# Kernel tuning notes

Hardware: AMD Instinct MI355X
Metric: run time of the kernel (lower is better)

Reference implementation:

```python
import jax, jax.numpy as jnp
import numpy as np

WEIGHT = 1.0  # init kwarg `weight`
BOX = 5      # half-size of the text box in pixels


def setup_inputs() -> dict:
    key = jax.random.key(0)
    k1, k2, k3, k4 = jax.random.split(key, 4)
    B, C, H, W, T = 32, 4, 512, 512, 64
    return {
        "predicted_noise": jax.random.normal(k1, (B, C, H, W), dtype=jnp.float32),
        "target_noise": jax.random.normal(k2, (B, C, H, W), dtype=jnp.float32),
        "text_tokens": jax.random.randint(k3, (B, T), 0, 50000, dtype=jnp.int64),
        "text_positions": jax.random.uniform(k4, (B, T, 2), dtype=jnp.float32),
    }


def _text_mask(text_positions, H, W, dtype):
    # text_positions: [B, T, 2] normalized (x, y). A valid token (x>0, y>0)
    # paints a [y_pos-5, y_pos+5) x [x_pos-5, x_pos+5) box of ones (clipped to image).
    x = text_positions[..., 0]
    y = text_positions[..., 1]
    valid = (x > 0) & (y > 0)                              # [B, T]
    x_pos = jnp.floor(x * W).astype(jnp.int32)             # int(x*W), x>0 so floor==trunc
    y_pos = jnp.floor(y * H).astype(jnp.int32)
    ii = jnp.arange(H, dtype=jnp.int32)                    # rows; clipping is implicit
    jj = jnp.arange(W, dtype=jnp.int32)
    cond_y = valid[..., None] & (ii >= y_pos[..., None] - BOX) & (ii < y_pos[..., None] + BOX)  # [B,T,H]
    cond_x = (jj >= x_pos[..., None] - BOX) & (jj < x_pos[..., None] + BOX)                      # [B,T,W]
    # union over tokens of the outer-product boxes, via a small matmul over T
    hits = jnp.einsum('bti,btj->bij', cond_y.astype(dtype), cond_x.astype(dtype))  # [B,H,W]
    return (hits > 0).astype(dtype)


def reference(predicted_noise, target_noise, text_tokens, text_positions):
    diff2 = (predicted_noise - target_noise) ** 2
    base_loss = jnp.mean(diff2)
    _, _, H, W = predicted_noise.shape
    mask = _text_mask(text_positions, H, W, predicted_noise.dtype)   # [B,H,W]
    text_weight = 1.0 + 3.0 * mask[:, None, :, :]                    # [B,1,H,W]
    text_loss = jnp.mean(text_weight * diff2)
    return base_loss + WEIGHT * (text_loss - base_loss)
```

## Files before the change

### kernel.cpp

```cpp
#include <hip/hip_runtime.h>

#define Bb 32
#define Cc 4
#define Hh 512
#define Ww 512
#define Tt 64
#define HW (Hh * Ww)
#define NTOT ((long long)Bb * Cc * Hh * Ww)
#define NVEC (NTOT / 4)
#define BLOCK 256
#define UNROLL 16
#define GRID (NVEC / (BLOCK * UNROLL))

#define ROWMASK_OFF 65536

__global__ __launch_bounds__(256) void build_rowmask_kernel(
    const float* __restrict__ pos,
    unsigned long long* __restrict__ rowmask)
{
    int b   = blockIdx.x;
    int tid = threadIdx.x;

    __shared__ int s_ylo[Tt], s_yhi[Tt], s_xlo[Tt], s_xhi[Tt];
    if (tid < Tt) {
        const float2 xy = ((const float2*)pos)[b * Tt + tid];
        bool valid = (xy.x > 0.0f) && (xy.y > 0.0f);
        int xp = (int)floorf(xy.x * (float)Ww);
        int yp = (int)floorf(xy.y * (float)Hh);
        int xlo = xp - 5; if (xlo < 0) xlo = 0;
        int xhi = xp + 5; if (xhi > Ww) xhi = Ww;
        if (!valid) { xlo = 0; xhi = 0; }
        s_ylo[tid] = valid ? yp - 5 : (1 << 30);
        s_yhi[tid] = valid ? yp + 5 : -(1 << 30);
        s_xlo[tid] = xlo;
        s_xhi[tid] = xhi;
    }
    __syncthreads();

#pragma unroll
    for (int r = 0; r < 2; ++r) {
        int h = 2 * tid + r;
        unsigned long long m[8];
#pragma unroll
        for (int i = 0; i < 8; ++i) m[i] = 0ull;

        for (int t = 0; t < Tt; ++t) {
            if (h < s_ylo[t] || h >= s_yhi[t]) continue;
            int xlo = s_xlo[t], xhi = s_xhi[t];
            if (xlo >= xhi) continue;
            int w0 = xlo >> 6;
            int w1 = (xhi - 1) >> 6;
            for (int wd = w0; wd <= w1; ++wd) {
                int lo = xlo - (wd << 6); if (lo < 0) lo = 0;
                int hi = xhi - (wd << 6); if (hi > 64) hi = 64;
                m[wd] |= (((1ull << (hi - lo)) - 1ull) << lo);
            }
        }

        ulonglong2* out = (ulonglong2*)(rowmask + ((size_t)b * Hh + h) * 8);
#pragma unroll
        for (int i = 0; i < 4; ++i)
            out[i] = make_ulonglong2(m[2 * i], m[2 * i + 1]);
    }
}

__global__ __launch_bounds__(256) void weighted_sq_sum_kernel(
    const float4* __restrict__ pred4,
    const float4* __restrict__ targ4,
    const unsigned long long* __restrict__ rowmask,
    double* __restrict__ partials)
{
    const int tid = threadIdx.x;
    const int g0  = blockIdx.x * (BLOCK * UNROLL) + tid;

    float4 A[UNROLL], Bv[UNROLL];
    unsigned long long Wd[UNROLL];

#pragma unroll
    for (int i = 0; i < UNROLL; ++i)
        A[i] = pred4[g0 + i * BLOCK];
#pragma unroll
    for (int i = 0; i < UNROLL; ++i)
        Bv[i] = targ4[g0 + i * BLOCK];
#pragma unroll
    for (int i = 0; i < UNROLL; ++i) {
        unsigned int e = (unsigned int)(g0 + i * BLOCK) << 2;
        unsigned int widx = ((e >> 20) << 12) | (((e >> 9) & 511u) << 3) |
                            ((e >> 6) & 7u);
        Wd[i] = rowmask[widx];
    }

    float sfull = 0.f, smask = 0.f;
#pragma unroll
    for (int i = 0; i < UNROLL; ++i) {
        float dx = A[i].x - Bv[i].x;
        float dy = A[i].y - Bv[i].y;
        float dz = A[i].z - Bv[i].z;
        float dw = A[i].w - Bv[i].w;
        float sx = dx * dx, sy = dy * dy, sz = dz * dz, sw = dw * dw;
        sfull += sx + sy + sz + sw;
        int shf = (int)(((unsigned int)(g0 + i * BLOCK) << 2) & 63u);
        unsigned long long word = Wd[i] >> shf;
        smask += (word & 1ull) ? sx : 0.f;
        smask += ((word >> 1) & 1ull) ? sy : 0.f;
        smask += ((word >> 2) & 1ull) ? sz : 0.f;
        smask += ((word >> 3) & 1ull) ? sw : 0.f;
    }

    double v = (double)sfull + 3.0 * (double)smask;

#pragma unroll
    for (int off = 32; off > 0; off >>= 1)
        v += __shfl_down(v, off, 64);

    __shared__ double lsum[4];
    int lane = tid & 63;
    int wid  = tid >> 6;
    if (lane == 0) lsum[wid] = v;
    __syncthreads();
    if (tid == 0)
        partials[blockIdx.x] = lsum[0] + lsum[1] + lsum[2] + lsum[3];
}

__global__ __launch_bounds__(256) void final_reduce_kernel(
    const double* __restrict__ partials, float* __restrict__ out)
{
    double t[GRID / BLOCK];
#pragma unroll
    for (int i = 0; i < GRID / BLOCK; ++i)
        t[i] = partials[i * BLOCK + threadIdx.x];
    double v = 0.0;
#pragma unroll
    for (int i = 0; i < GRID / BLOCK; ++i) v += t[i];

#pragma unroll
    for (int off = 32; off > 0; off >>= 1)
        v += __shfl_down(v, off, 64);
    __shared__ double lsum[4];
    int lane = threadIdx.x & 63;
    int wid  = threadIdx.x >> 6;
    if (lane == 0) lsum[wid] = v;
    __syncthreads();
    if (threadIdx.x == 0)
        out[0] = (float)((lsum[0] + lsum[1] + lsum[2] + lsum[3]) *
                         (1.0 / (double)NTOT));
}

extern "C" void kernel_launch(void* const* d_in, const int* in_sizes, int n_in,
                              void* d_out, int out_size, void* d_ws, size_t ws_size,
                              hipStream_t stream) {
    const float4* pred = (const float4*)d_in[0];
    const float4* targ = (const float4*)d_in[1];
    const float* pos   = (const float*)d_in[3];

    double* partials = (double*)d_ws;
    unsigned long long* rowmask =
        (unsigned long long*)((char*)d_ws + ROWMASK_OFF);
    float* out = (float*)d_out;

    build_rowmask_kernel<<<Bb, BLOCK, 0, stream>>>(pos, rowmask);
    weighted_sq_sum_kernel<<<GRID, BLOCK, 0, stream>>>(pred, targ, rowmask,
                                                       partials);
    final_reduce_kernel<<<1, 256, 0, stream>>>(partials, out);
}
```

Baseline: 299.1 us.

## Split into unmasked streaming sum via LDS DMA plus sparse masked-pixel pass

```diff
diff --git a/kernel.cpp b/kernel.cpp
--- a/kernel.cpp
+++ b/kernel.cpp
@@ -7,12 +7,22 @@
 #define Tt 64
 #define HW (Hh * Ww)
 #define NTOT ((long long)Bb * Cc * Hh * Ww)
-#define NVEC (NTOT / 4)
+#define HOT_GRID 2048
 #define BLOCK 256
-#define UNROLL 16
-#define GRID (NVEC / (BLOCK * UNROLL))
-
-#define ROWMASK_OFF 65536
+#define NBATCH 8
+#define BATCH_B 2048
+#define WAVE_BYTES (NBATCH * BATCH_B)
+#define NWAVES (HOT_GRID * 4)
+
+#define MPART_OFF   65536
+#define ROWMASK_OFF 73728
+#define NMPART 256
+
+#define WAITCNT_VM4 0x0F74
+#define WAITCNT_VM0 0x0F70
+
+typedef const __attribute__((address_space(1))) unsigned int* gptr_t;
+typedef __attribute__((address_space(3))) unsigned int* lptr_t;
 
 __global__ __launch_bounds__(256) void build_rowmask_kernel(
     const float* __restrict__ pos,
@@ -64,84 +74,124 @@
     }
 }
 
-__global__ __launch_bounds__(256) void weighted_sq_sum_kernel(
-    const float4* __restrict__ pred4,
-    const float4* __restrict__ targ4,
-    const unsigned long long* __restrict__ rowmask,
-    double* __restrict__ partials)
-{
-    const int tid = threadIdx.x;
-    const int g0  = blockIdx.x * (BLOCK * UNROLL) + tid;
-
-    float4 A[UNROLL], Bv[UNROLL];
-    unsigned long long Wd[UNROLL];
-
-#pragma unroll
-    for (int i = 0; i < UNROLL; ++i)
-        A[i] = pred4[g0 + i * BLOCK];
-#pragma unroll
-    for (int i = 0; i < UNROLL; ++i)
-        Bv[i] = targ4[g0 + i * BLOCK];
-#pragma unroll
-    for (int i = 0; i < UNROLL; ++i) {
-        unsigned int e = (unsigned int)(g0 + i * BLOCK) << 2;
-        unsigned int widx = ((e >> 20) << 12) | (((e >> 9) & 511u) << 3) |
-                            ((e >> 6) & 7u);
-        Wd[i] = rowmask[widx];
-    }
-
-    float sfull = 0.f, smask = 0.f;
-#pragma unroll
-    for (int i = 0; i < UNROLL; ++i) {
-        float dx = A[i].x - Bv[i].x;
-        float dy = A[i].y - Bv[i].y;
-        float dz = A[i].z - Bv[i].z;
-        float dw = A[i].w - Bv[i].w;
-        float sx = dx * dx, sy = dy * dy, sz = dz * dz, sw = dw * dw;
-        sfull += sx + sy + sz + sw;
-        int shf = (int)(((unsigned int)(g0 + i * BLOCK) << 2) & 63u);
-        unsigned long long word = Wd[i] >> shf;
-        smask += (word & 1ull) ? sx : 0.f;
-        smask += ((word >> 1) & 1ull) ? sy : 0.f;
-        smask += ((word >> 2) & 1ull) ? sz : 0.f;
-        smask += ((word >> 3) & 1ull) ? sw : 0.f;
-    }
-
-    double v = (double)sfull + 3.0 * (double)smask;
-
+__global__ __launch_bounds__(256) void stream_sq_sum_kernel(
+    const char* __restrict__ pred,
+    const char* __restrict__ targ,
+    double* __restrict__ wpartials)
+{
+    __shared__ char smem[4 * 8192];
+    const int tid  = threadIdx.x;
+    const int lane = tid & 63;
+    const int wid  = tid >> 6;
+    const int W    = blockIdx.x * 4 + wid;
+
+    const char* pbase = pred + (size_t)W * WAVE_BYTES;
+    const char* tbase = targ + (size_t)W * WAVE_BYTES;
+    char* my = smem + wid * 8192;
+
+    auto issue_batch = [&](int batch) {
+        const int bo = (batch & 1) * 4096;
+        const char* p = pbase + batch * BATCH_B;
+        const char* t = tbase + batch * BATCH_B;
+#pragma unroll
+        for (int j = 0; j < 2; ++j)
+            __builtin_amdgcn_global_load_lds(
+                (gptr_t)(p + j * 1024 + lane * 16),
+                (lptr_t)(my + bo + j * 1024), 16, 0, 0);
+#pragma unroll
+        for (int j = 0; j < 2; ++j)
+            __builtin_amdgcn_global_load_lds(
+                (gptr_t)(t + j * 1024 + lane * 16),
+                (lptr_t)(my + bo + 2048 + j * 1024), 16, 0, 0);
+    };
+
+    issue_batch(0);
+    issue_batch(1);
+
+    float sfull = 0.f;
+#pragma unroll
+    for (int i = 0; i < NBATCH; ++i) {
+        if (i == NBATCH - 1) __builtin_amdgcn_s_waitcnt(WAITCNT_VM0);
+        else                 __builtin_amdgcn_s_waitcnt(WAITCNT_VM4);
+
+        const int bo = (i & 1) * 4096;
+        float4 a0 = *(const float4*)(my + bo +    0 + lane * 16);
+        float4 a1 = *(const float4*)(my + bo + 1024 + lane * 16);
+        float4 b0 = *(const float4*)(my + bo + 2048 + lane * 16);
+        float4 b1 = *(const float4*)(my + bo + 3072 + lane * 16);
+
+        float dx, dy, dz, dw;
+        dx = a0.x - b0.x; dy = a0.y - b0.y; dz = a0.z - b0.z; dw = a0.w - b0.w;
+        sfull += dx * dx; sfull += dy * dy; sfull += dz * dz; sfull += dw * dw;
+        dx = a1.x - b1.x; dy = a1.y - b1.y; dz = a1.z - b1.z; dw = a1.w - b1.w;
+        sfull += dx * dx; sfull += dy * dy; sfull += dz * dz; sfull += dw * dw;
+
+        if (i + 2 < NBATCH) issue_batch(i + 2);
+    }
+
+    double v = (double)sfull;
 #pragma unroll
     for (int off = 32; off > 0; off >>= 1)
         v += __shfl_down(v, off, 64);
-
+    if (lane == 0) wpartials[W] = v;
+}
+
+__global__ __launch_bounds__(256) void masked_sum_kernel(
+    const float* __restrict__ pred,
+    const float* __restrict__ targ,
+    const unsigned long long* __restrict__ rowmask,
+    double* __restrict__ mpartials)
+{
+    int row = blockIdx.x * 256 + threadIdx.x;
+    int b = row >> 9;
+    int h = row & 511;
+
+    const unsigned long long* rm = rowmask + (size_t)row * 8;
+    const float* pb = pred + (size_t)b * (Cc * HW) + (size_t)h * Ww;
+    const float* tb = targ + (size_t)b * (Cc * HW) + (size_t)h * Ww;
+
+    float acc = 0.f;
+#pragma unroll
+    for (int w = 0; w < 8; ++w) {
+        unsigned long long word = rm[w];
+        while (word) {
+            int bit = __builtin_ctzll(word);
+            word &= word - 1;
+            int c = (w << 6) + bit;
+            float d0 = pb[0 * HW + c] - tb[0 * HW + c];
+            float d1 = pb[1 * HW + c] - tb[1 * HW + c];
+            float d2 = pb[2 * HW + c] - tb[2 * HW + c];
+            float d3 = pb[3 * HW + c] - tb[3 * HW + c];
+            acc += d0 * d0 + d1 * d1 + d2 * d2 + d3 * d3;
+        }
+    }
+
+    double v = (double)acc;
+#pragma unroll
+    for (int off = 32; off > 0; off >>= 1)
+        v += __shfl_down(v, off, 64);
+    if ((threadIdx.x & 63) == 0)
+        mpartials[blockIdx.x * 4 + (threadIdx.x >> 6)] = v;
+}
+
+__global__ __launch_bounds__(256) void final_reduce_kernel(
+    const double* __restrict__ wpartials,
+    const double* __restrict__ mpartials,
+    float* __restrict__ out)
+{
+    int tid = threadIdx.x;
+    double v = 0.0;
+    for (int i = tid; i < NWAVES; i += 256) v += wpartials[i];
+    double m = mpartials[tid];
+    double t = v + 3.0 * m;
+
+#pragma unroll
+    for (int off = 32; off > 0; off >>= 1)
+        t += __shfl_down(t, off, 64);
     __shared__ double lsum[4];
-    int lane = tid & 63;
-    int wid  = tid >> 6;
-    if (lane == 0) lsum[wid] = v;
+    if ((tid & 63) == 0) lsum[tid >> 6] = t;
     __syncthreads();
     if (tid == 0)
-        partials[blockIdx.x] = lsum[0] + lsum[1] + lsum[2] + lsum[3];
-}
-
-__global__ __launch_bounds__(256) void final_reduce_kernel(
-    const double* __restrict__ partials, float* __restrict__ out)
-{
-    double t[GRID / BLOCK];
-#pragma unroll
-    for (int i = 0; i < GRID / BLOCK; ++i)
-        t[i] = partials[i * BLOCK + threadIdx.x];
-    double v = 0.0;
-#pragma unroll
-    for (int i = 0; i < GRID / BLOCK; ++i) v += t[i];
-
-#pragma unroll
-    for (int off = 32; off > 0; off >>= 1)
-        v += __shfl_down(v, off, 64);
-    __shared__ double lsum[4];
-    int lane = threadIdx.x & 63;
-    int wid  = threadIdx.x >> 6;
-    if (lane == 0) lsum[wid] = v;
-    __syncthreads();
-    if (threadIdx.x == 0)
         out[0] = (float)((lsum[0] + lsum[1] + lsum[2] + lsum[3]) *
                          (1.0 / (double)NTOT));
 }
@@ -149,17 +199,19 @@
 extern "C" void kernel_launch(void* const* d_in, const int* in_sizes, int n_in,
                               void* d_out, int out_size, void* d_ws, size_t ws_size,
                               hipStream_t stream) {
-    const float4* pred = (const float4*)d_in[0];
-    const float4* targ = (const float4*)d_in[1];
+    const char*  pred  = (const char*)d_in[0];
+    const char*  targ  = (const char*)d_in[1];
     const float* pos   = (const float*)d_in[3];
 
-    double* partials = (double*)d_ws;
+    double* wpartials = (double*)d_ws;
+    double* mpartials = (double*)((char*)d_ws + MPART_OFF);
     unsigned long long* rowmask =
         (unsigned long long*)((char*)d_ws + ROWMASK_OFF);
     float* out = (float*)d_out;
 
     build_rowmask_kernel<<<Bb, BLOCK, 0, stream>>>(pos, rowmask);
-    weighted_sq_sum_kernel<<<GRID, BLOCK, 0, stream>>>(pred, targ, rowmask,
-                                                       partials);
-    final_reduce_kernel<<<1, 256, 0, stream>>>(partials, out);
-}
+    stream_sq_sum_kernel<<<HOT_GRID, BLOCK, 0, stream>>>(pred, targ, wpartials);
+    masked_sum_kernel<<<Bb * Hh / 256, BLOCK, 0, stream>>>(
+        (const float*)pred, (const float*)targ, rowmask, mpartials);
+    final_reduce_kernel<<<1, 256, 0, stream>>>(wpartials, mpartials, out);
+}
```

Measured after the change: 339.5 us. 1.14x slower.
